# Performance work log

Hardware: AMD Instinct MI355X
Metric: run time of the kernel (lower is better)

Reference implementation:

```python
import jax, jax.numpy as jnp
import numpy as np

N = 50000      # nodes
E = 800000     # edges (avg degree 16)
IN, HID, OUT = 256, 128, 64
K, ALPHA = 4, 0.0  # APPNPConv(k=4, alpha=0.0)


def setup_inputs() -> dict:
    key = jax.random.key(0)
    ks = jax.random.split(key, 5)
    features = jax.random.normal(ks[0], (N, IN), jnp.float32)
    src = jax.random.randint(ks[1], (E,), 0, N, jnp.int32)
    dst = jax.random.randint(ks[2], (E,), 0, N, jnp.int32)
    W1 = jax.random.normal(ks[3], (IN, HID), jnp.float32) / np.float32(np.sqrt(IN))
    b1 = jnp.zeros((HID,), jnp.float32)
    W3 = jax.random.normal(ks[4], (HID, OUT), jnp.float32) / np.float32(np.sqrt(HID))
    b3 = jnp.zeros((OUT,), jnp.float32)
    return dict(features=features, src=src, dst=dst, W1=W1, b1=b1, W3=W3, b3=b3)


def _sym_norms(src, dst, n):
    # D_out^{-1/2} for source side, D_in^{-1/2} for destination side (DGL norm='both')
    ones = jnp.ones((src.shape[0],), jnp.float32)
    deg_out = jax.ops.segment_sum(ones, src, num_segments=n)
    deg_in = jax.ops.segment_sum(ones, dst, num_segments=n)
    return jnp.clip(deg_out, 1.0) ** -0.5, jnp.clip(deg_in, 1.0) ** -0.5


def _prop(x, src, dst, norm_src, norm_dst):
    # x: [N, D]. Symmetric-normalized SpMM: D_in^{-1/2} A D_out^{-1/2} x
    msg = (x * norm_src[:, None])[src]                       # [E, D] gather
    agg = jax.ops.segment_sum(msg, dst, num_segments=x.shape[0])  # [N, D] scatter-add
    return agg * norm_dst[:, None]


def reference(features, src, dst, W1, b1, W3, b3):
    ns, nd = _sym_norms(src, dst, N)
    # GraphConv 1 (weight-first since in_dim > hidden_dim; math identical either way)
    h = _prop(features @ W1, src, dst, ns, nd) + b1
    # dropout is identity in eval mode (training=False)
    # APPNPConv: k=4 power-iteration steps with teleport alpha=0.0
    h0 = h
    for _ in range(K):
        h = (1.0 - ALPHA) * _prop(h, src, dst, ns, nd) + ALPHA * h0
    # GraphConv 3
    out = _prop(h @ W3, src, dst, ns, nd) + b3
    return out
```

## Files before the change

kernel.cpp:

```cpp
#include <hip/hip_runtime.h>
#include <math.h>

#define N_NODES 50000
#define N_EDGES 800000
#define DIN 256
#define DHID 128
#define DOUT 64
#define CSTRIDE 64
#define ZROW N_NODES
#define HBLOCKS 256
#define HCHUNK (N_EDGES / HBLOCKS)
#define HWORDS (N_NODES / 4)


__global__ void k_hist(const int* __restrict__ idx, unsigned int* __restrict__ partials) {
    __shared__ unsigned int h[HWORDS];
    int t = threadIdx.x;
    for (int w = t; w < HWORDS; w += 256) h[w] = 0u;
    __syncthreads();
    int base = blockIdx.x * HCHUNK;
    for (int i = t; i < HCHUNK; i += 256) {
        int s = idx[base + i];
        atomicAdd(&h[s >> 2], 1u << ((s & 3) << 3));
    }
    __syncthreads();
    unsigned int* outp = partials + (size_t)blockIdx.x * HWORDS;
    for (int w = t; w < HWORDS; w += 256) outp[w] = h[w];
}

__global__ void k_hreduce(const unsigned int* __restrict__ partials, int* __restrict__ deg) {
    int wid = blockIdx.x * 256 + threadIdx.x;
    if (wid >= HWORDS) return;
    unsigned int s0 = 0, s1 = 0, s2 = 0, s3 = 0;
#pragma unroll 4
    for (int b = 0; b < HBLOCKS; ++b) {
        unsigned int w = partials[(size_t)b * HWORDS + wid];
        s0 += w & 0xffu; s1 += (w >> 8) & 0xffu;
        s2 += (w >> 16) & 0xffu; s3 += w >> 24;
    }
    int4 o; o.x = (int)s0; o.y = (int)s1; o.z = (int)s2; o.w = (int)s3;
    *(int4*)(deg + (wid << 2)) = o;
}

__global__ void k_hprefix(const unsigned int* __restrict__ partials,
                          unsigned int* __restrict__ prefix, int* __restrict__ deg) {
    int wid = blockIdx.x * 256 + threadIdx.x;
    if (wid >= HWORDS) return;
    unsigned int run = 0;
    for (int b = 0; b < HBLOCKS; ++b) {
        unsigned int w = partials[(size_t)b * HWORDS + wid];
        prefix[(size_t)b * HWORDS + wid] = run;
        run += w;
    }
    int4 o;
    o.x = (int)(run & 0xffu); o.y = (int)((run >> 8) & 0xffu);
    o.z = (int)((run >> 16) & 0xffu); o.w = (int)(run >> 24);
    *(int4*)(deg + (wid << 2)) = o;
}

__global__ void k_fill(const int* __restrict__ src, const int* __restrict__ dst,
                       const unsigned int* __restrict__ prefix,
                       unsigned short* __restrict__ csr) {
    __shared__ unsigned int h[HWORDS];
    int t = threadIdx.x;
    const unsigned int* prow = prefix + (size_t)blockIdx.x * HWORDS;
    for (int w = t; w < HWORDS; w += 256) h[w] = prow[w];
    __syncthreads();
    int base = blockIdx.x * HCHUNK;
    for (int i = t; i < HCHUNK; i += 256) {
        int s = src[base + i], d = dst[base + i];
        int sh = (d & 3) << 3;
        unsigned int old = atomicAdd(&h[d >> 2], 1u << sh);
        int slot = (int)((old >> sh) & 0xffu);
        csr[(d << 6) + slot] = (unsigned short)s;
    }
}

__global__ void k_norms(const int* __restrict__ deg_out, const int* __restrict__ deg_in,
                        float* ns, float* nd, float* c,
                        unsigned short* __restrict__ csr, int n) {
    int i = blockIdx.x * 256 + threadIdx.x;
    if (i < n) {
        int dov = deg_out[i]; if (dov < 1) dov = 1;
        int div_ = deg_in[i]; if (div_ < 1) div_ = 1;
        float a = 1.0f / sqrtf((float)dov);
        float b = 1.0f / sqrtf((float)div_);
        ns[i] = a; nd[i] = b; c[i] = a * b;
        int di = deg_in[i];
        int npad = (di + 7) & ~7;
        for (int p = di; p < npad; ++p) csr[(i << 6) + p] = (unsigned short)ZROW;
    }
}


__global__ void k_weights(const float* __restrict__ W1, const float* __restrict__ b1,
                          const float* __restrict__ W3,
                          float* __restrict__ W13, float* __restrict__ bb,
                          float* __restrict__ Y0, float* __restrict__ Y1) {
    if (blockIdx.x == 65) {
        int t = threadIdx.x;
        if (t < DOUT) {
            Y0[((size_t)ZROW << 6) + t] = 0.f;
            Y1[((size_t)ZROW << 6) + t] = 0.f;
        }
        return;
    }
    if (blockIdx.x == 64) {
        int j = threadIdx.x;
        if (j < DOUT) {
            float s = 0.f;
            for (int k = 0; k < DHID; ++k) s += b1[k] * W3[k * DOUT + j];
            bb[j] = s;
        }
        return;
    }
    int idx = blockIdx.x * 256 + threadIdx.x;
    int i = idx >> 6, j = idx & 63;
    float s = 0.f;
    for (int k = 0; k < DHID; ++k) s += W1[i * DHID + k] * W3[k * DOUT + j];
    W13[idx] = s;
}


__global__ void k_gemm(const float* __restrict__ X, const float* __restrict__ W13,
                       const float* __restrict__ ns, float* __restrict__ Y) {
    __shared__ float As[16][68];
    __shared__ float Bs[16][64];
    int tid = threadIdx.x;
    int tx = tid & 15, ty = tid >> 4;
    int row0 = blockIdx.x * 64;
    float acc[4][4];
#pragma unroll
    for (int i = 0; i < 4; ++i)
#pragma unroll
        for (int j = 0; j < 4; ++j) acc[i][j] = 0.f;

    int lr = tid >> 2;
    int lk = (tid & 3) << 2;
    int arow = row0 + lr;
    if (arow > N_NODES - 1) arow = N_NODES - 1;

    for (int k0 = 0; k0 < DIN; k0 += 16) {
        float4 a = *(const float4*)(X + (size_t)arow * DIN + k0 + lk);
        As[lk + 0][lr] = a.x; As[lk + 1][lr] = a.y;
        As[lk + 2][lr] = a.z; As[lk + 3][lr] = a.w;
        float4 b = *(const float4*)(W13 + (size_t)(k0 + (tid >> 4)) * DOUT + ((tid & 15) << 2));
        *(float4*)&Bs[tid >> 4][(tid & 15) << 2] = b;
        __syncthreads();
#pragma unroll
        for (int k = 0; k < 16; ++k) {
            float4 av = *(const float4*)&As[k][ty << 2];
            float4 bv = *(const float4*)&Bs[k][tx << 2];
            float ar[4] = {av.x, av.y, av.z, av.w};
            float br[4] = {bv.x, bv.y, bv.z, bv.w};
#pragma unroll
            for (int i = 0; i < 4; ++i)
#pragma unroll
                for (int j = 0; j < 4; ++j) acc[i][j] += ar[i] * br[j];
        }
        __syncthreads();
    }
#pragma unroll
    for (int i = 0; i < 4; ++i) {
        int row = row0 + (ty << 2) + i;
        if (row < N_NODES) {
            float nsr = ns[row];
            float4 o;
            o.x = acc[i][0] * nsr; o.y = acc[i][1] * nsr;
            o.z = acc[i][2] * nsr; o.w = acc[i][3] * nsr;
            *(float4*)(Y + (size_t)row * DOUT + (tx << 2)) = o;
        }
    }
}


template <int MODE>
__global__ void k_spmm(const float* __restrict__ x, float* __restrict__ y,
                       const unsigned short* __restrict__ csr,
                       const int* __restrict__ cnt,
                       const float* __restrict__ c, const float* __restrict__ ns,
                       const float* __restrict__ nd,
                       const float* __restrict__ bb, const float* __restrict__ b3) {
    int node = blockIdx.x * 4 + (threadIdx.x >> 6);
    int lane = threadIdx.x & 63;
    int npad = (cnt[node] + 7) & ~7;
    int sv = csr[(node << 6) + lane];
    const float* xl = x + lane;
    float acc = 0.f;
    for (int j = 0; j < npad; j += 8) {
        int a0 = __builtin_amdgcn_readlane(sv, j);
        int a1 = __builtin_amdgcn_readlane(sv, j + 1);
        int a2 = __builtin_amdgcn_readlane(sv, j + 2);
        int a3 = __builtin_amdgcn_readlane(sv, j + 3);
        int a4 = __builtin_amdgcn_readlane(sv, j + 4);
        int a5 = __builtin_amdgcn_readlane(sv, j + 5);
        int a6 = __builtin_amdgcn_readlane(sv, j + 6);
        int a7 = __builtin_amdgcn_readlane(sv, j + 7);
        float t0 = xl[(size_t)a0 << 6];
        float t1 = xl[(size_t)a1 << 6];
        float t2 = xl[(size_t)a2 << 6];
        float t3 = xl[(size_t)a3 << 6];
        float t4 = xl[(size_t)a4 << 6];
        float t5 = xl[(size_t)a5 << 6];
        float t6 = xl[(size_t)a6 << 6];
        float t7 = xl[(size_t)a7 << 6];
        acc += t0; acc += t1; acc += t2; acc += t3;
        acc += t4; acc += t5; acc += t6; acc += t7;
    }
    float r;
    if (MODE == 0)      r = c[node] * acc + ns[node] * bb[lane];
    else if (MODE == 1) r = c[node] * acc;
    else                r = nd[node] * acc + b3[lane];
    y[(node << 6) + lane] = r;
}


extern "C" void kernel_launch(void* const* d_in, const int* in_sizes, int n_in,
                              void* d_out, int out_size, void* d_ws, size_t ws_size,
                              hipStream_t stream) {
    const float* X   = (const float*)d_in[0];
    const int*   src = (const int*)d_in[1];
    const int*   dst = (const int*)d_in[2];
    const float* W1  = (const float*)d_in[3];
    const float* b1  = (const float*)d_in[4];
    const float* W3  = (const float*)d_in[5];
    const float* b3  = (const float*)d_in[6];
    float* out = (float*)d_out;

    char* ws = (char*)d_ws;
    size_t off = 0;
    auto alloc = [&](size_t bytes) -> void* {
        void* p = ws + off;
        off = (off + bytes + 255) & ~(size_t)255;
        return p;
    };
    const size_t BIGSZ = (size_t)(N_NODES + 1) * DOUT * 4;
    char* bufA = (char*)alloc(BIGSZ);
    char* bufB = (char*)alloc(BIGSZ);
    int*            deg_out = (int*)alloc((size_t)N_NODES * 4);
    int*            deg_in  = (int*)alloc((size_t)N_NODES * 4);
    unsigned short* csr     = (unsigned short*)alloc((size_t)N_NODES * CSTRIDE * 2);
    float*          ns      = (float*)alloc((size_t)N_NODES * 4);
    float*          nd      = (float*)alloc((size_t)N_NODES * 4);
    float*          cc      = (float*)alloc((size_t)N_NODES * 4);
    float*          W13     = (float*)alloc((size_t)DIN * DOUT * 4);
    float*          bb      = (float*)alloc(DOUT * 4);

    unsigned int* pS   = (unsigned int*)bufA;
    unsigned int* pD   = (unsigned int*)bufB;
    unsigned int* pref = (unsigned int*)bufA;
    float*        Y0   = (float*)bufB;
    float*        Y1   = (float*)bufA;

    const int nblk = (N_NODES + 255) / 256;
    const int hblk = (HWORDS + 255) / 256;

    k_hist<<<HBLOCKS, 256, 0, stream>>>(src, pS);
    k_hreduce<<<hblk, 256, 0, stream>>>(pS, deg_out);
    k_hist<<<HBLOCKS, 256, 0, stream>>>(dst, pD);
    k_hprefix<<<hblk, 256, 0, stream>>>(pD, pref, deg_in);
    k_fill<<<HBLOCKS, 256, 0, stream>>>(src, dst, pref, csr);
    k_norms<<<nblk, 256, 0, stream>>>(deg_out, deg_in, ns, nd, cc, csr, N_NODES);

    k_weights<<<66, 256, 0, stream>>>(W1, b1, W3, W13, bb, Y0, Y1);

    k_gemm<<<(N_NODES + 63) / 64, 256, 0, stream>>>(X, W13, ns, Y0);

    k_spmm<0><<<N_NODES / 4, 256, 0, stream>>>(Y0, Y1, csr, deg_in, cc, ns, nd, bb, b3);
    k_spmm<1><<<N_NODES / 4, 256, 0, stream>>>(Y1, Y0, csr, deg_in, cc, ns, nd, bb, b3);
    k_spmm<1><<<N_NODES / 4, 256, 0, stream>>>(Y0, Y1, csr, deg_in, cc, ns, nd, bb, b3);
    k_spmm<1><<<N_NODES / 4, 256, 0, stream>>>(Y1, Y0, csr, deg_in, cc, ns, nd, bb, b3);
    k_spmm<1><<<N_NODES / 4, 256, 0, stream>>>(Y0, Y1, csr, deg_in, cc, ns, nd, bb, b3);
    k_spmm<2><<<N_NODES / 4, 256, 0, stream>>>(Y1, out, csr, deg_in, cc, ns, nd, bb, b3);
}
```

Measured before the change: 350.4 us.

## Fuse degree reduction, prefix and norms; bitonic-sort CSR rows per node

Merges the out-degree reduction, the in-degree prefix scan and the normalisation into one kernel, so two launches go away and the separate deg_out buffer is dropped. It also replaces the padding kernel with a wavefront-wide bitonic sort of each node's 64-slot neighbour list. Empty slots are filled with the zero-row index, so each row's source indices are ascending. Sorted gathers in the six SpMM passes should hit nearby rows and improve cache locality, at the cost of an extra shuffle-heavy sort pass over all nodes.

```diff
diff --git a/kernel.cpp b/kernel.cpp
--- a/kernel.cpp
+++ b/kernel.cpp
@@ -28,34 +28,47 @@
     for (int w = t; w < HWORDS; w += 256) outp[w] = h[w];
 }
 
-__global__ void k_hreduce(const unsigned int* __restrict__ partials, int* __restrict__ deg) {
+__global__ void k_hpre(const unsigned int* __restrict__ pS,
+                       const unsigned int* __restrict__ pD,
+                       unsigned int* __restrict__ prefix,
+                       int* __restrict__ deg_in,
+                       float* __restrict__ ns, float* __restrict__ nd,
+                       float* __restrict__ cc) {
     int wid = blockIdx.x * 256 + threadIdx.x;
     if (wid >= HWORDS) return;
-    unsigned int s0 = 0, s1 = 0, s2 = 0, s3 = 0;
+    unsigned int o0 = 0, o1 = 0, o2 = 0, o3 = 0;
 #pragma unroll 4
     for (int b = 0; b < HBLOCKS; ++b) {
-        unsigned int w = partials[(size_t)b * HWORDS + wid];
-        s0 += w & 0xffu; s1 += (w >> 8) & 0xffu;
-        s2 += (w >> 16) & 0xffu; s3 += w >> 24;
-    }
-    int4 o; o.x = (int)s0; o.y = (int)s1; o.z = (int)s2; o.w = (int)s3;
-    *(int4*)(deg + (wid << 2)) = o;
-}
-
-__global__ void k_hprefix(const unsigned int* __restrict__ partials,
-                          unsigned int* __restrict__ prefix, int* __restrict__ deg) {
-    int wid = blockIdx.x * 256 + threadIdx.x;
-    if (wid >= HWORDS) return;
+        unsigned int w = pS[(size_t)b * HWORDS + wid];
+        o0 += w & 0xffu; o1 += (w >> 8) & 0xffu;
+        o2 += (w >> 16) & 0xffu; o3 += w >> 24;
+    }
     unsigned int run = 0;
     for (int b = 0; b < HBLOCKS; ++b) {
-        unsigned int w = partials[(size_t)b * HWORDS + wid];
+        unsigned int w = pD[(size_t)b * HWORDS + wid];
         prefix[(size_t)b * HWORDS + wid] = run;
         run += w;
     }
-    int4 o;
-    o.x = (int)(run & 0xffu); o.y = (int)((run >> 8) & 0xffu);
-    o.z = (int)((run >> 16) & 0xffu); o.w = (int)(run >> 24);
-    *(int4*)(deg + (wid << 2)) = o;
+    unsigned int i0 = run & 0xffu, i1 = (run >> 8) & 0xffu;
+    unsigned int i2 = (run >> 16) & 0xffu, i3 = run >> 24;
+    int4 di; di.x = (int)i0; di.y = (int)i1; di.z = (int)i2; di.w = (int)i3;
+    *(int4*)(deg_in + (wid << 2)) = di;
+
+    unsigned int dov[4] = {o0, o1, o2, o3};
+    unsigned int div_[4] = {i0, i1, i2, i3};
+    float4 vns, vnd, vcc;
+    float* pns = &vns.x; float* pnd = &vnd.x; float* pcc = &vcc.x;
+#pragma unroll
+    for (int q = 0; q < 4; ++q) {
+        unsigned int a = dov[q] < 1u ? 1u : dov[q];
+        unsigned int b = div_[q] < 1u ? 1u : div_[q];
+        float fa = 1.0f / sqrtf((float)a);
+        float fb = 1.0f / sqrtf((float)b);
+        pns[q] = fa; pnd[q] = fb; pcc[q] = fa * fb;
+    }
+    *(float4*)(ns + (wid << 2)) = vns;
+    *(float4*)(nd + (wid << 2)) = vnd;
+    *(float4*)(cc + (wid << 2)) = vcc;
 }
 
 __global__ void k_fill(const int* __restrict__ src, const int* __restrict__ dst,
@@ -76,20 +89,25 @@
     }
 }
 
-__global__ void k_norms(const int* __restrict__ deg_out, const int* __restrict__ deg_in,
-                        float* ns, float* nd, float* c,
-                        unsigned short* __restrict__ csr, int n) {
-    int i = blockIdx.x * 256 + threadIdx.x;
-    if (i < n) {
-        int dov = deg_out[i]; if (dov < 1) dov = 1;
-        int div_ = deg_in[i]; if (div_ < 1) div_ = 1;
-        float a = 1.0f / sqrtf((float)dov);
-        float b = 1.0f / sqrtf((float)div_);
-        ns[i] = a; nd[i] = b; c[i] = a * b;
-        int di = deg_in[i];
-        int npad = (di + 7) & ~7;
-        for (int p = di; p < npad; ++p) csr[(i << 6) + p] = (unsigned short)ZROW;
-    }
+__global__ void k_sortpad(unsigned short* __restrict__ csr,
+                          const int* __restrict__ deg_in) {
+    int node = blockIdx.x * 4 + (threadIdx.x >> 6);
+    int lane = threadIdx.x & 63;
+    int deg = deg_in[node];
+    int v = csr[(node << 6) + lane];
+    if (lane >= deg) v = ZROW;
+#pragma unroll
+    for (int k = 2; k <= 64; k <<= 1) {
+        for (int j = k >> 1; j > 0; j >>= 1) {
+            int other = __shfl_xor(v, j);
+            bool up = ((lane & k) == 0);
+            bool lower = ((lane & j) == 0);
+            int mn = v < other ? v : other;
+            int mx = v < other ? other : v;
+            v = (lower == up) ? mn : mx;
+        }
+    }
+    csr[(node << 6) + lane] = (unsigned short)v;
 }
 
 
@@ -237,7 +255,6 @@
     const size_t BIGSZ = (size_t)(N_NODES + 1) * DOUT * 4;
     char* bufA = (char*)alloc(BIGSZ);
     char* bufB = (char*)alloc(BIGSZ);
-    int*            deg_out = (int*)alloc((size_t)N_NODES * 4);
     int*            deg_in  = (int*)alloc((size_t)N_NODES * 4);
     unsigned short* csr     = (unsigned short*)alloc((size_t)N_NODES * CSTRIDE * 2);
     float*          ns      = (float*)alloc((size_t)N_NODES * 4);
@@ -252,15 +269,13 @@
     float*        Y0   = (float*)bufB;
     float*        Y1   = (float*)bufA;
 
-    const int nblk = (N_NODES + 255) / 256;
     const int hblk = (HWORDS + 255) / 256;
 
     k_hist<<<HBLOCKS, 256, 0, stream>>>(src, pS);
-    k_hreduce<<<hblk, 256, 0, stream>>>(pS, deg_out);
     k_hist<<<HBLOCKS, 256, 0, stream>>>(dst, pD);
-    k_hprefix<<<hblk, 256, 0, stream>>>(pD, pref, deg_in);
+    k_hpre<<<hblk, 256, 0, stream>>>(pS, pD, pref, deg_in, ns, nd, cc);
     k_fill<<<HBLOCKS, 256, 0, stream>>>(src, dst, pref, csr);
-    k_norms<<<nblk, 256, 0, stream>>>(deg_out, deg_in, ns, nd, cc, csr, N_NODES);
+    k_sortpad<<<N_NODES / 4, 256, 0, stream>>>(csr, deg_in);
 
     k_weights<<<66, 256, 0, stream>>>(W1, b1, W3, W13, bb, Y0, Y1);
 
```

Measured after the change: 364.0 us. +3.9%, slower.
